# Optimization experiments

Measured on AMD Instinct MI355X. Metric: run time of the kernel, lower is better.

Reference implementation:

```python
import jax, jax.numpy as jnp
import numpy as np

TEMPERATURE = 0.05
EPS = 1e-8  # matches torch F.cosine_similarity eps default


def setup_inputs() -> dict:
    key = jax.random.key(0)
    k1, k2 = jax.random.split(key)
    N, D = 8192, 512
    query_embeddings = jax.random.normal(k1, (N, D), dtype=jnp.float32)
    pos_embeddings = jax.random.normal(k2, (N, D), dtype=jnp.float32)
    return {"query_embeddings": query_embeddings, "pos_embeddings": pos_embeddings}


def reference(query_embeddings, pos_embeddings):
    # cosine_similarity(q[:,None,:], p[None,:,:], dim=2) == normalize(q) @ normalize(p).T
    qn = query_embeddings / jnp.maximum(
        jnp.linalg.norm(query_embeddings, axis=-1, keepdims=True), EPS)
    pn = pos_embeddings / jnp.maximum(
        jnp.linalg.norm(pos_embeddings, axis=-1, keepdims=True), EPS)
    sim = jnp.einsum('nd,md->nm', qn, pn) / TEMPERATURE  # [N, N] logits
    # cross-entropy with targets = arange(N): diagonal logits are the positives
    logz = jax.nn.logsumexp(sim, axis=-1)               # [N]
    diag = jnp.diagonal(sim)                             # [N]
    loss = jnp.mean(logz - diag)
    return loss
```

## Files before the change

kernel.cpp:

```cpp
#include <hip/hip_runtime.h>
#include <hip/hip_bf16.h>

#define NROWS 8192
#define DIM 512
#define BM 256
#define BN 256

typedef int   i32x4 __attribute__((ext_vector_type(4)));
typedef int   i32x8 __attribute__((ext_vector_type(8)));
typedef float f32x4 __attribute__((ext_vector_type(4)));

#define FP8_SCALE_1 0x7f7f7f7f

__global__ __launch_bounds__(256) void prep_k(
    const float* __restrict__ q, const float* __restrict__ p,
    char* __restrict__ qf, char* __restrict__ pf,
    float* __restrict__ diag) {
  __shared__ char ldsq[16 * 528];
  __shared__ char ldsp[16 * 528];
  const int tid = threadIdx.x;
  const int blk = blockIdx.x;
  const int rr = tid >> 4;
  const int cs = tid & 15;
  const int i  = blk * 16 + rr;
  const float4* qr = (const float4*)(q + (size_t)i * DIM);
  const float4* pr = (const float4*)(p + (size_t)i * DIM);

  float4 qv[8], pv[8];
  float ssq = 0.0f, ssp = 0.0f, dt = 0.0f;
  #pragma unroll
  for (int jj = 0; jj < 8; ++jj) {
    qv[jj] = qr[jj * 16 + cs];
    pv[jj] = pr[jj * 16 + cs];
    ssq += qv[jj].x*qv[jj].x + qv[jj].y*qv[jj].y + qv[jj].z*qv[jj].z + qv[jj].w*qv[jj].w;
    ssp += pv[jj].x*pv[jj].x + pv[jj].y*pv[jj].y + pv[jj].z*pv[jj].z + pv[jj].w*pv[jj].w;
    dt  += qv[jj].x*pv[jj].x + qv[jj].y*pv[jj].y + qv[jj].z*pv[jj].z + qv[jj].w*pv[jj].w;
  }
  #pragma unroll
  for (int m = 1; m < 16; m <<= 1) {
    ssq += __shfl_xor(ssq, m, 64);
    ssp += __shfl_xor(ssp, m, 64);
    dt  += __shfl_xor(dt,  m, 64);
  }
  const float invq = 1.0f / fmaxf(sqrtf(ssq), 1e-8f);
  const float invp = 1.0f / fmaxf(sqrtf(ssp), 1e-8f);
  if (cs == 0) diag[i] = dt * invq * invp * 20.0f;

  #pragma unroll
  for (int jj = 0; jj < 8; ++jj) {
    int rq = 0, rp = 0;
    rq = __builtin_amdgcn_cvt_pk_fp8_f32(qv[jj].x * invq, qv[jj].y * invq, rq, false);
    rq = __builtin_amdgcn_cvt_pk_fp8_f32(qv[jj].z * invq, qv[jj].w * invq, rq, true);
    rp = __builtin_amdgcn_cvt_pk_fp8_f32(pv[jj].x * invp, pv[jj].y * invp, rp, false);
    rp = __builtin_amdgcn_cvt_pk_fp8_f32(pv[jj].z * invp, pv[jj].w * invp, rp, true);
    *(unsigned int*)(ldsq + rr * 528 + jj * 64 + cs * 4) = (unsigned int)rq;
    *(unsigned int*)(ldsp + rr * 528 + jj * 64 + cs * 4) = (unsigned int)rp;
  }
  __syncthreads();

  const int panel = blk >> 4, rg = blk & 15;
  #pragma unroll
  for (int u = 0; u < 2; ++u) {
    const int o = 2 * tid + u;
    const int kt = o >> 7, sel = (o >> 6) & 1, laneT = o & 63;
    const int rrs = laneT & 15;
    const int srcoff = kt * 128 + (laneT >> 4) * 32 + sel * 16;
    const i32x4 va = *(const i32x4*)(ldsq + rrs * 528 + srcoff);
    const size_t aaddr =
        ((((size_t)(panel * 4 + kt) * 2 + (rg >> 3)) * 8 + (rg & 7)) * 2 + sel) * 1024
        + laneT * 16;
    *(i32x4*)(qf + aaddr) = va;
    const i32x4 vb = *(const i32x4*)(ldsp + rrs * 528 + srcoff);
    const size_t baddr =
        ((((size_t)(panel * 4 + kt) * 4 + (rg >> 2)) * 4 + (rg & 3)) * 2 + sel) * 1024
        + laneT * 16;
    *(i32x4*)(pf + baddr) = vb;
  }
}

__global__ __launch_bounds__(512, 2) void gemm_lse_k(
    const char* __restrict__ qf, const char* __restrict__ pf,
    float* __restrict__ partial) {
  __shared__ float psum[1024];
  const int tid = threadIdx.x;
  const int lane = tid & 63, wid = tid >> 6;
  const int wr = wid >> 2, wc = wid & 3;
  const int l15 = lane & 15, l4 = lane >> 4;
  const int b = blockIdx.x;
  const int g = b & 7;
  const int j = b >> 3;
  const int panelA = (g & 3) * 8 + (j & 7);
  const int bnset  = (g >> 2) * 16 + (j >> 3) * 2;
  const int bm = panelA * BM;
  const char* aPanel = qf + (size_t)panelA * 131072 + (size_t)lane * 16;
  const char* pBase  = pf + (size_t)lane * 16;

  f32x4 acc[4][8] = {};
  i32x8 af[8], bf[4];

  #pragma unroll 1
  for (int tt = 0; tt < 8; ++tt) {
    const int kt = tt & 3, t = tt >> 2;
    const char* aB = aPanel + (size_t)(kt * 2 + wr) * 16384;
    const char* bB = pBase +
        (size_t)(((bnset + t) * 4 + kt) * 4 + wc) * 8192;

    #pragma unroll
    for (int mf = 0; mf < 8; ++mf) {
      const i32x4 lo = *(const i32x4*)(aB + mf * 2048);
      const i32x4 hi = *(const i32x4*)(aB + mf * 2048 + 1024);
      af[mf] = __builtin_shufflevector(lo, hi, 0, 1, 2, 3, 4, 5, 6, 7);
    }
    #pragma unroll
    for (int nf = 0; nf < 4; ++nf) {
      const i32x4 lo = *(const i32x4*)(bB + nf * 2048);
      const i32x4 hi = *(const i32x4*)(bB + nf * 2048 + 1024);
      bf[nf] = __builtin_shufflevector(lo, hi, 0, 1, 2, 3, 4, 5, 6, 7);
    }

    __builtin_amdgcn_s_setprio(1);
    #pragma unroll
    for (int nb = 0; nb < 4; ++nb)
      #pragma unroll
      for (int am = 0; am < 8; ++am)
        acc[nb][am] = __builtin_amdgcn_mfma_scale_f32_16x16x128_f8f6f4(
            bf[nb], af[am], acc[nb][am], 0, 0, 0, FP8_SCALE_1, 0, FP8_SCALE_1);
    __builtin_amdgcn_s_setprio(0);

    if ((tt & 3) == 3) {
      const int bxc = bnset + t;
      #pragma unroll
      for (int am = 0; am < 8; ++am) {
        float s = 0.0f;
        #pragma unroll
        for (int nb = 0; nb < 4; ++nb)
          #pragma unroll
          for (int r = 0; r < 4; ++r)
            s += __expf(acc[nb][am][r] * 20.0f - 20.0f);
        s += __shfl_xor(s, 16, 64);
        s += __shfl_xor(s, 32, 64);
        if (l4 == 0)
          psum[wc * 256 + wr * 128 + am * 16 + l15] = s;
      }
      __syncthreads();
      if (tid < 256)
        partial[(size_t)(bm + tid) * 32 + bxc] =
            psum[tid] + psum[256 + tid] + psum[512 + tid] + psum[768 + tid];
      __syncthreads();
      #pragma unroll
      for (int nb = 0; nb < 4; ++nb)
        #pragma unroll
        for (int am = 0; am < 8; ++am)
          acc[nb][am] = f32x4{0.0f, 0.0f, 0.0f, 0.0f};
    }
  }
}

__global__ __launch_bounds__(256) void rowloss_k(
    const float* __restrict__ partial, const float* __restrict__ diag,
    float* __restrict__ rowloss) {
  const int i = blockIdx.x * 256 + threadIdx.x;
  const float4* pr = (const float4*)(partial + (size_t)i * 32);
  float s = 0.0f;
  #pragma unroll
  for (int c = 0; c < 8; ++c) {
    const float4 v = pr[c];
    s += v.x + v.y + v.z + v.w;
  }
  rowloss[i] = __logf(s) + 20.0f - diag[i];
}

__global__ __launch_bounds__(1024) void final_k(
    const float* __restrict__ rowloss, float* __restrict__ out) {
  const int t = threadIdx.x;
  float s = 0.0f;
  #pragma unroll
  for (int j = 0; j < 8; ++j) s += rowloss[t + j * 1024];
  #pragma unroll
  for (int m = 1; m < 64; m <<= 1) s += __shfl_xor(s, m, 64);
  __shared__ float red[16];
  if ((t & 63) == 0) red[t >> 6] = s;
  __syncthreads();
  if (t == 0) {
    float acc = 0.0f;
    #pragma unroll
    for (int w = 0; w < 16; ++w) acc += red[w];
    out[0] = acc * (1.0f / (float)NROWS);
  }
}

extern "C" void kernel_launch(void* const* d_in, const int* in_sizes, int n_in,
                              void* d_out, int out_size, void* d_ws, size_t ws_size,
                              hipStream_t stream) {
  const float* q = (const float*)d_in[0];
  const float* p = (const float*)d_in[1];
  char* w = (char*)d_ws;
  char* qf = w;
  char* pf = w + 4194304;
  float* partial    = (float*)(w + 8388608);
  float* diag       = (float*)(w + 9437184);
  float* rowloss    = (float*)(w + 9437184 + 32768);
  float* out = (float*)d_out;

  prep_k<<<NROWS / 16, 256, 0, stream>>>(q, p, qf, pf, diag);
  gemm_lse_k<<<512, 512, 0, stream>>>(qf, pf, partial);
  rowloss_k<<<NROWS / 256, 256, 0, stream>>>(partial, diag, rowloss);
  final_k<<<1, 1024, 0, stream>>>(rowloss, out);
}
```

Before: 58.18 us.

## Stage Q panel through swizzled LDS with double-buffered async loads, halve grid

The Q operand is now written row-major by prep and streamed into LDS with global_load_lds, using an XOR swizzle and double buffering across k-steps. Each block now covers four column tiles instead of two, so the grid shrinks from 512 to 256 blocks and each block reuses its A panel across more N tiles. This cuts redundant global reads of A, but adds a barrier on every iteration, uses about 68KB of LDS, and leaves fewer blocks to fill the device.

```diff
diff --git a/kernel.cpp b/kernel.cpp
--- a/kernel.cpp
+++ b/kernel.cpp
@@ -12,11 +12,17 @@
 
 #define FP8_SCALE_1 0x7f7f7f7f
 
+__device__ __forceinline__ void gld_lds16(const void* g, void* l) {
+  __builtin_amdgcn_global_load_lds(
+      (__attribute__((address_space(1))) unsigned int*)(g),
+      (__attribute__((address_space(3))) unsigned int*)(l),
+      16, 0, 0);
+}
+
 __global__ __launch_bounds__(256) void prep_k(
     const float* __restrict__ q, const float* __restrict__ p,
     char* __restrict__ qf, char* __restrict__ pf,
     float* __restrict__ diag) {
-  __shared__ char ldsq[16 * 528];
   __shared__ char ldsp[16 * 528];
   const int tid = threadIdx.x;
   const int blk = blockIdx.x;
@@ -53,7 +59,7 @@
     rq = __builtin_amdgcn_cvt_pk_fp8_f32(qv[jj].z * invq, qv[jj].w * invq, rq, true);
     rp = __builtin_amdgcn_cvt_pk_fp8_f32(pv[jj].x * invp, pv[jj].y * invp, rp, false);
     rp = __builtin_amdgcn_cvt_pk_fp8_f32(pv[jj].z * invp, pv[jj].w * invp, rp, true);
-    *(unsigned int*)(ldsq + rr * 528 + jj * 64 + cs * 4) = (unsigned int)rq;
+    *(unsigned int*)(qf + (size_t)i * 512 + jj * 64 + cs * 4) = (unsigned int)rq;
     *(unsigned int*)(ldsp + rr * 528 + jj * 64 + cs * 4) = (unsigned int)rp;
   }
   __syncthreads();
@@ -65,11 +71,6 @@
     const int kt = o >> 7, sel = (o >> 6) & 1, laneT = o & 63;
     const int rrs = laneT & 15;
     const int srcoff = kt * 128 + (laneT >> 4) * 32 + sel * 16;
-    const i32x4 va = *(const i32x4*)(ldsq + rrs * 528 + srcoff);
-    const size_t aaddr =
-        ((((size_t)(panel * 4 + kt) * 2 + (rg >> 3)) * 8 + (rg & 7)) * 2 + sel) * 1024
-        + laneT * 16;
-    *(i32x4*)(qf + aaddr) = va;
     const i32x4 vb = *(const i32x4*)(ldsp + rrs * 528 + srcoff);
     const size_t baddr =
         ((((size_t)(panel * 4 + kt) * 4 + (rg >> 2)) * 4 + (rg & 3)) * 2 + sel) * 1024
@@ -78,54 +79,91 @@
   }
 }
 
+__device__ __forceinline__ i32x8 rd32(const char* base, int c0, int sw) {
+  const i32x4 lo = *(const i32x4*)(base + ((c0     ) ^ sw));
+  const i32x4 hi = *(const i32x4*)(base + ((c0 + 16) ^ sw));
+  return __builtin_shufflevector(lo, hi, 0, 1, 2, 3, 4, 5, 6, 7);
+}
+__device__ __forceinline__ void stage_half(const char* __restrict__ g, char* dstb,
+                                           int rowbase, int h, int tid, int kb) {
+  #pragma unroll
+  for (int j = 0; j < 2; ++j) {
+    const int idx = j * 512 + tid;
+    const int rl = idx >> 3;
+    const int scb = ((idx & 7) << 4) ^ ((rl & 7) << 4);
+    gld_lds16(g + (size_t)(rowbase + h * 128 + rl) * 512 + kb + scb,
+              dstb + h * 16384 + idx * 16);
+  }
+}
+
 __global__ __launch_bounds__(512, 2) void gemm_lse_k(
     const char* __restrict__ qf, const char* __restrict__ pf,
     float* __restrict__ partial) {
-  __shared__ float psum[1024];
+  __shared__ __attribute__((aligned(16))) char lds[69632];
   const int tid = threadIdx.x;
   const int lane = tid & 63, wid = tid >> 6;
   const int wr = wid >> 2, wc = wid & 3;
   const int l15 = lane & 15, l4 = lane >> 4;
+  const int sw = (l15 & 7) << 4;
+  const int c0 = l4 * 32;
   const int b = blockIdx.x;
   const int g = b & 7;
   const int j = b >> 3;
-  const int panelA = (g & 3) * 8 + (j & 7);
-  const int bnset  = (g >> 2) * 16 + (j >> 3) * 2;
-  const int bm = panelA * BM;
-  const char* aPanel = qf + (size_t)panelA * 131072 + (size_t)lane * 16;
-  const char* pBase  = pf + (size_t)lane * 16;
+  const int bm = ((g & 3) * 8 + (j & 7)) * BM;
+  const int bnset = (g >> 2) * 16 + (j >> 3) * 4;
+  float* psum = (float*)(lds + 65536);
+  const int aOff = wr * 16384 + l15 * 128;
+  const char* pBase = pf + (size_t)lane * 16;
 
   f32x4 acc[4][8] = {};
-  i32x8 af[8], bf[4];
+  i32x8 af0[4], af1[4], bf[4];
+
+  stage_half(qf, lds, bm, 0, tid, 0);
+  stage_half(qf, lds, bm, 1, tid, 0);
+  asm volatile("s_waitcnt vmcnt(0)" ::: "memory");
+  __builtin_amdgcn_s_barrier();
 
   #pragma unroll 1
-  for (int tt = 0; tt < 8; ++tt) {
+  for (int tt = 0; tt < 16; ++tt) {
     const int kt = tt & 3, t = tt >> 2;
-    const char* aB = aPanel + (size_t)(kt * 2 + wr) * 16384;
-    const char* bB = pBase +
-        (size_t)(((bnset + t) * 4 + kt) * 4 + wc) * 8192;
-
-    #pragma unroll
-    for (int mf = 0; mf < 8; ++mf) {
-      const i32x4 lo = *(const i32x4*)(aB + mf * 2048);
-      const i32x4 hi = *(const i32x4*)(aB + mf * 2048 + 1024);
-      af[mf] = __builtin_shufflevector(lo, hi, 0, 1, 2, 3, 4, 5, 6, 7);
-    }
+    char* rb = lds + (tt & 1) * 32768;
+    char* sb = lds + ((tt + 1) & 1) * 32768;
+    const int kbn = ((tt + 1) & 3) * 128;
+
+    const char* bB = pBase + (size_t)(((bnset + t) * 4 + kt) * 4 + wc) * 8192;
     #pragma unroll
     for (int nf = 0; nf < 4; ++nf) {
       const i32x4 lo = *(const i32x4*)(bB + nf * 2048);
       const i32x4 hi = *(const i32x4*)(bB + nf * 2048 + 1024);
       bf[nf] = __builtin_shufflevector(lo, hi, 0, 1, 2, 3, 4, 5, 6, 7);
     }
+    #pragma unroll
+    for (int mf = 0; mf < 4; ++mf)
+      af0[mf] = rd32(rb + aOff + mf * 2048, c0, sw);
+    #pragma unroll
+    for (int mf = 0; mf < 4; ++mf)
+      af1[mf] = rd32(rb + aOff + 8192 + mf * 2048, c0, sw);
+    if (tt < 15) {
+      stage_half(qf, sb, bm, 0, tid, kbn);
+      stage_half(qf, sb, bm, 1, tid, kbn);
+    }
 
     __builtin_amdgcn_s_setprio(1);
     #pragma unroll
-    for (int nb = 0; nb < 4; ++nb)
-      #pragma unroll
-      for (int am = 0; am < 8; ++am)
-        acc[nb][am] = __builtin_amdgcn_mfma_scale_f32_16x16x128_f8f6f4(
-            bf[nb], af[am], acc[nb][am], 0, 0, 0, FP8_SCALE_1, 0, FP8_SCALE_1);
+    for (int nb = 0; nb < 4; ++nb) {
+      #pragma unroll
+      for (int mf = 0; mf < 4; ++mf)
+        acc[nb][mf] = __builtin_amdgcn_mfma_scale_f32_16x16x128_f8f6f4(
+            bf[nb], af0[mf], acc[nb][mf], 0, 0, 0, FP8_SCALE_1, 0, FP8_SCALE_1);
+      #pragma unroll
+      for (int mf = 0; mf < 4; ++mf)
+        acc[nb][4 + mf] = __builtin_amdgcn_mfma_scale_f32_16x16x128_f8f6f4(
+            bf[nb], af1[mf], acc[nb][4 + mf], 0, 0, 0, FP8_SCALE_1, 0, FP8_SCALE_1);
+    }
     __builtin_amdgcn_s_setprio(0);
+
+    asm volatile("s_waitcnt vmcnt(0)" ::: "memory");
+    __builtin_amdgcn_s_barrier();
 
     if ((tt & 3) == 3) {
       const int bxc = bnset + t;
@@ -142,11 +180,11 @@
         if (l4 == 0)
           psum[wc * 256 + wr * 128 + am * 16 + l15] = s;
       }
-      __syncthreads();
+      asm volatile("s_waitcnt lgkmcnt(0)" ::: "memory");
+      __builtin_amdgcn_s_barrier();
       if (tid < 256)
         partial[(size_t)(bm + tid) * 32 + bxc] =
             psum[tid] + psum[256 + tid] + psum[512 + tid] + psum[768 + tid];
-      __syncthreads();
       #pragma unroll
       for (int nb = 0; nb < 4; ++nb)
         #pragma unroll
@@ -203,7 +241,7 @@
   float* out = (float*)d_out;
 
   prep_k<<<NROWS / 16, 256, 0, stream>>>(q, p, qf, pf, diag);
-  gemm_lse_k<<<512, 512, 0, stream>>>(qf, pf, partial);
+  gemm_lse_k<<<256, 512, 0, stream>>>(qf, pf, partial);
   rowloss_k<<<NROWS / 256, 256, 0, stream>>>(partial, diag, rowloss);
   final_k<<<1, 1024, 0, stream>>>(rowloss, out);
 }
```

After: 60.23 us. 1.04x slower.
